# Performance work log

Hardware: AMD Instinct MI355X
Metric: run time of the kernel (lower is better)

Reference implementation:

```python
import jax, jax.numpy as jnp
import numpy as np

EPS = 1e-5

def inorm(x):
    # instance norm over time (last) axis; torch.std is unbiased (ddof=1)
    m = jnp.mean(x, axis=-1, keepdims=True)
    s = jnp.sqrt(jnp.var(x, axis=-1, ddof=1, keepdims=True))
    return (x - m) / (s + EPS)

def tinorm(x):
    # time-wise instance norm: normalize over channel axis (dim=1)
    m = jnp.mean(x, axis=1, keepdims=True)
    s = jnp.sqrt(jnp.var(x, axis=1, ddof=1, keepdims=True))
    return (x - m) / (s + EPS)

def adaptive_norm(src, trg, wq, wk, wv, norm_fn):
    # src, trg: [B,C,T]; wq/wk/wv: [out,in] as in nn.Linear
    temp = src.shape[1] ** 0.5
    q = jnp.einsum('bct,oc->bto', norm_fn(src), wq)        # [B,Ts,C]
    k = jnp.einsum('bct,oc->bto', norm_fn(trg), wk)        # [B,Tt,C]
    v = jnp.einsum('bct,oc->bto', trg, wv)                 # [B,Tt,C]
    attn = jax.nn.softmax(jnp.einsum('bsc,btc->bst', q / temp, k), axis=-1)
    mean = jnp.einsum('bst,btc->bsc', attn, v)             # attn-weighted mean
    var = jax.nn.relu(jnp.einsum('bst,btc->bsc', attn, v * v) - mean * mean)
    mean_c = jnp.mean(mean, axis=1)[:, :, None]            # [B,C,1]
    std_c = jnp.sqrt(jnp.mean(var, axis=1))[:, :, None]    # [B,C,1]
    return std_c * inorm(src) + mean_c

def sap(x, w, b):
    # self-attention pooling over axis 1; x: [B,N,C], w: [C], b: [1]
    a = jax.nn.softmax(jnp.einsum('bnc,c->bn', x, w) + b, axis=-1)
    return jnp.einsum('bnc,bn->bc', x, a)

def setup_inputs():
    key = jax.random.key(0)
    ks = jax.random.split(key, 24)
    B, C, Ts, Tt, S = 4, 512, 2048, 2048, 2048
    sc = 1.0 / np.sqrt(C).astype(np.float32)
    return {
        'src': jax.random.normal(ks[0], (B, C, Ts), jnp.float32),
        'trg': jax.random.normal(ks[1], (B, C, Tt), jnp.float32),
        'means': jax.random.normal(ks[2], (B, S, C), jnp.float32),
        'stds': jax.random.uniform(ks[3], (B, S, C), jnp.float32),
        'wq_t': jax.random.normal(ks[4], (C, C), jnp.float32) * sc,
        'wk_t': jax.random.normal(ks[5], (C, C), jnp.float32) * sc,
        'wv_t': jax.random.normal(ks[6], (C, C), jnp.float32) * sc,
        'wq_c': jax.random.normal(ks[7], (C, C), jnp.float32) * sc,
        'wk_c': jax.random.normal(ks[8], (C, C), jnp.float32) * sc,
        'wv_c': jax.random.normal(ks[9], (C, C), jnp.float32) * sc,
        'conv1_w': jax.random.normal(ks[10], (C, 2 * C), jnp.float32) * sc,
        'conv1_b': jax.random.normal(ks[11], (C,), jnp.float32) * 0.02,
        'conv2_w': jax.random.normal(ks[12], (C, C, 3), jnp.float32) * sc,
        'bn_g': jax.random.uniform(ks[13], (C,), jnp.float32, 0.5, 1.5),
        'bn_b': jax.random.normal(ks[14], (C,), jnp.float32) * 0.05,
        'bn_m': jax.random.normal(ks[15], (C,), jnp.float32) * 0.1,
        'bn_v': jax.random.uniform(ks[16], (C,), jnp.float32, 0.5, 1.5),
        'msap_w': jax.random.normal(ks[17], (C,), jnp.float32) * sc,
        'msap_b': jax.random.normal(ks[18], (1,), jnp.float32) * 0.02,
        'ssap_w': jax.random.normal(ks[19], (C,), jnp.float32) * sc,
        'ssap_b': jax.random.normal(ks[20], (1,), jnp.float32) * 0.02,
    }

def reference(src, trg, means, stds, wq_t, wk_t, wv_t, wq_c, wk_c, wv_c,
              conv1_w, conv1_b, conv2_w, bn_g, bn_b, bn_m, bn_v,
              msap_w, msap_b, ssap_w, ssap_b):
    src1 = adaptive_norm(src, trg, wq_t, wk_t, wv_t, tinorm)   # TAN
    src2 = adaptive_norm(src, trg, wq_c, wk_c, wv_c, inorm)    # CAN
    x = jnp.concatenate([src1, src2], axis=1)                  # [B,2C,T]
    # conv1: kernel_size=1 -> pointwise GEMM
    x = jnp.einsum('bct,oc->bot', x, conv1_w) + conv1_b[None, :, None]
    # conv2: Conv1d(k=3, pad=1, bias=False) + BatchNorm1d(eval) + ReLU
    x = jax.lax.conv_general_dilated(x, conv2_w, (1,), 'SAME',
                                     dimension_numbers=('NCH', 'OIH', 'NCH'))
    x = (x - bn_m[None, :, None]) * jax.lax.rsqrt(bn_v[None, :, None] + EPS)
    x = x * bn_g[None, :, None] + bn_b[None, :, None]
    x = jax.nn.relu(x)
    # GLAN
    mean = sap(means, msap_w, msap_b)[:, :, None]              # [B,C,1]
    std = sap(stds, ssap_w, ssap_b)[:, :, None]                # [B,C,1]
    return inorm(x) * std + mean
```

## Files before the change

kernel.cpp:

```cpp
#include <hip/hip_runtime.h>
#include <cstdint>
#include <cstddef>

#define B_ 4
#define C_ 512
#define T_ 2048
#define S_ 2048
#define EPSF 1e-5f

typedef __bf16 bf16;
typedef __attribute__((ext_vector_type(8))) __bf16 bf16x8;
typedef __attribute__((ext_vector_type(4))) float f32x4;

__device__ __forceinline__ bf16 f2b(float f){ return (bf16)f; }
__device__ __forceinline__ float b2f(bf16 h){ return (float)h; }

__device__ __forceinline__ void gl_lds16(const void* g, void* l){
  __builtin_amdgcn_global_load_lds((__attribute__((address_space(1))) void*)(g),
                                   (__attribute__((address_space(3))) void*)(l), 16, 0, 0);
}

__device__ __forceinline__ float wave_sum(float v){
#pragma unroll
  for (int o = 32; o; o >>= 1) v += __shfl_xor(v, o, 64);
  return v;
}
__device__ __forceinline__ float wave_max(float v){
#pragma unroll
  for (int o = 32; o; o >>= 1) v = fmaxf(v, __shfl_xor(v, o, 64));
  return v;
}

template<int EPI, int TNW, int SWZ>
__global__ void __launch_bounds__(256) gemm_nt(
    const bf16* __restrict__ A, const bf16* __restrict__ Bm, void* __restrict__ Cout,
    int K, int lda, int ldb, int ldc,
    long long sA, long long sB, long long sC, long long sCb,
    int zdivA, int zmodB, int nblk, float scale,
    const float* __restrict__ rs, const float* __restrict__ rsh,
    const float* __restrict__ cbias,
    float* __restrict__ osum, float* __restrict__ osum2, long long sRs)
{
  constexpr int TN = TNW*32;
  __shared__ alignas(16) bf16 lA[128*64];
  __shared__ alignas(16) bf16 lB[TN*64];
  __shared__ float l_sh[EPI == 3 ? 128 : 4];
  const int tid = threadIdx.x;
  int z, m0, n0;
  if (SWZ) {
    const int id = blockIdx.x;
    z = id & 7;
    const int r = id >> 3;
    n0 = (r % nblk) * TN;
    m0 = (r / nblk) * 128;
  } else {
    z = blockIdx.z; m0 = blockIdx.y*128; n0 = blockIdx.x*TN;
  }
  const bf16* Ab = A + (long long)(z / zdivA) * sA;
  const bf16* Bb = Bm + (long long)(z % zmodB) * sB;
  const int lane = tid & 63, wvi = tid >> 6;
  const int wm = wvi >> 1, wn = wvi & 1;

  f32x4 acc[4][TNW] = {};
  f32x4 accL[4] = {};
  bf16x8 vone;
#pragma unroll
  for (int j = 0; j < 8; ++j) vone[j] = f2b(1.f);

  const int lrow = tid >> 3;
  const int lcol = ((tid ^ lrow) & 7) * 8;
  const bf16* pa = Ab + (long long)(m0 + lrow)*lda + lcol;
  const bf16* pb = Bb + (long long)(n0 + lrow)*ldb + lcol;
  char* sa = (char*)lA + tid*16;
  char* sb = (char*)lB + tid*16;

  for (int k0 = 0; k0 < K; k0 += 64) {
#pragma unroll
    for (int it = 0; it < 4; ++it)
      gl_lds16(pa + (long long)it*32*lda + k0, sa + it*4096);
#pragma unroll
    for (int it = 0; it < TNW; ++it)
      gl_lds16(pb + (long long)it*32*ldb + k0, sb + it*4096);
    __syncthreads();
#pragma unroll
    for (int ks = 0; ks < 2; ++ks) {
      const int kq = ks*4 + (lane >> 4);
      bf16x8 af[4], bfr[TNW];
#pragma unroll
      for (int mt = 0; mt < 4; ++mt) {
        int r = wm*64 + mt*16 + (lane & 15);
        af[mt] = *(const bf16x8*)&lA[r*64 + ((kq ^ (r & 7))*8)];
      }
#pragma unroll
      for (int nt = 0; nt < TNW; ++nt) {
        int r = wn*(TNW*16) + nt*16 + (lane & 15);
        bfr[nt] = *(const bf16x8*)&lB[r*64 + ((kq ^ (r & 7))*8)];
      }
#pragma unroll
      for (int mt = 0; mt < 4; ++mt)
#pragma unroll
        for (int nt = 0; nt < TNW; ++nt)
          acc[mt][nt] = __builtin_amdgcn_mfma_f32_16x16x32_bf16(af[mt], bfr[nt], acc[mt][nt], 0, 0, 0);
      if (EPI == 3 && wn == 0) {
#pragma unroll
        for (int mt = 0; mt < 4; ++mt)
          accL[mt] = __builtin_amdgcn_mfma_f32_16x16x32_bf16(af[mt], vone, accL[mt], 0, 0, 0);
      }
    }
    __syncthreads();
  }

  if (EPI == 3) {
    if (wn == 0 && (lane & 15) == 0) {
#pragma unroll
      for (int mt = 0; mt < 4; ++mt)
#pragma unroll
        for (int i = 0; i < 4; ++i)
          l_sh[wm*64 + mt*16 + (lane >> 4)*4 + i] = accL[mt][i];
    }
    __syncthreads();
    if (n0 == 0 && tid < 128)
      ((float*)Cout)[(long long)z*sC + m0 + tid] = l_sh[tid];
    float linv[4][4];
#pragma unroll
    for (int mt = 0; mt < 4; ++mt)
#pragma unroll
      for (int i = 0; i < 4; ++i)
        linv[mt][i] = 1.f / l_sh[wm*64 + mt*16 + (lane >> 4)*4 + i];
    float* red1 = (float*)lA;
    float* red2 = red1 + 4*TNW*16;
    float s1[TNW], s2[TNW];
#pragma unroll
    for (int nt = 0; nt < TNW; ++nt) {
      s1[nt] = 0.f; s2[nt] = 0.f;
#pragma unroll
      for (int mt = 0; mt < 4; ++mt)
#pragma unroll
        for (int i = 0; i < 4; ++i) {
          float v = acc[mt][nt][i] * linv[mt][i];
          s1[nt] += v; s2[nt] += v*v;
        }
      s1[nt] += __shfl_xor(s1[nt], 16, 64);
      s1[nt] += __shfl_xor(s1[nt], 32, 64);
      s2[nt] += __shfl_xor(s2[nt], 16, 64);
      s2[nt] += __shfl_xor(s2[nt], 32, 64);
    }
    if (lane < 16) {
#pragma unroll
      for (int nt = 0; nt < TNW; ++nt) {
        red1[(wvi*TNW + nt)*16 + lane] = s1[nt];
        red2[(wvi*TNW + nt)*16 + lane] = s2[nt];
      }
    }
    __syncthreads();
    if (tid < 2*TN) {
      const int which = tid >= TN;
      const int col = tid - which*TN;
      const int wn2 = col / (TNW*16), rem = col % (TNW*16);
      const float* rr = which ? red2 : red1;
      float v = rr[wn2*(TNW*16) + rem] + rr[(2+wn2)*(TNW*16) + rem];
      float* dst = which ? osum2 : osum;
      atomicAdd(&dst[sCb*z + n0 + col], v);
    }
    return;
  }

  const int cr = (lane >> 4)*4, cc = lane & 15;
#pragma unroll
  for (int mt = 0; mt < 4; ++mt) {
#pragma unroll
    for (int i = 0; i < 4; ++i) {
      const int mm = m0 + wm*64 + mt*16 + cr + i;
      float rsum = 0.f, rsum2 = 0.f;
#pragma unroll
      for (int nt = 0; nt < TNW; ++nt) {
        const int nn = n0 + wn*(TNW*16) + nt*16 + cc;
        float v = acc[mt][nt][i];
        const long long co = sC*z + (long long)mm*ldc + nn;
        if (EPI == 0) {
          v *= scale;
          if (cbias) v += cbias[sCb*z + nn];
          ((bf16*)Cout)[co] = f2b(v);
        } else if (EPI == 2) {
          v = fmaxf(v*rs[mm] + rsh[mm], 0.f);
          ((float*)Cout)[co] = v;
          rsum += v; rsum2 += v*v;
        } else if (EPI == 5) {
          ((bf16*)Cout)[co] = f2b(__expf(v));
        }
      }
      if (EPI == 2) {
        rsum += __shfl_xor(rsum, 1, 64); rsum += __shfl_xor(rsum, 2, 64);
        rsum += __shfl_xor(rsum, 4, 64); rsum += __shfl_xor(rsum, 8, 64);
        rsum2 += __shfl_xor(rsum2, 1, 64); rsum2 += __shfl_xor(rsum2, 2, 64);
        rsum2 += __shfl_xor(rsum2, 4, 64); rsum2 += __shfl_xor(rsum2, 8, 64);
        if (cc == 0) {
          atomicAdd(&osum[(long long)z*sRs + mm], rsum);
          atomicAdd(&osum2[(long long)z*sRs + mm], rsum2);
        }
      }
    }
  }
}

__global__ void __launch_bounds__(256) instats_k(const float* __restrict__ src,
    const float* __restrict__ trg, float* __restrict__ inm, float* __restrict__ ins,
    float* __restrict__ tnm, float* __restrict__ tns)
{
  const int bid = blockIdx.x, tid = threadIdx.x;
  if (bid < 4096) {
    __shared__ float r1[4], r2[4];
    const int row = bid;
    const float* x = (row < B_*C_) ? src + (long long)row*T_
                                   : trg + (long long)(row - B_*C_)*T_;
    float s1 = 0.f, s2 = 0.f;
#pragma unroll
    for (int h = 0; h < 2; ++h) {
      f32x4 v = *(const f32x4*)(x + h*1024 + tid*4);
#pragma unroll
      for (int j = 0; j < 4; ++j){ s1 += v[j]; s2 += v[j]*v[j]; }
    }
    s1 = wave_sum(s1); s2 = wave_sum(s2);
    const int lane = tid & 63, w = tid >> 6;
    if (!lane){ r1[w] = s1; r2[w] = s2; }
    __syncthreads();
    if (tid == 0){
      s1 = r1[0]+r1[1]+r1[2]+r1[3];
      s2 = r2[0]+r2[1]+r2[2]+r2[3];
      float m = s1 * (1.f/T_);
      float var = (s2 - s1*m) * (1.f/(T_-1));
      inm[row] = m; ins[row] = sqrtf(fmaxf(var, 0.f));
    }
  } else {
    __shared__ float r1[4][64], r2[4][64];
    const int cid = bid - 4096;
    const int z = cid >> 5, t0 = (cid & 31)*64;
    const float* X = (z < B_) ? src : trg;
    const int b = z & (B_-1);
    const int tl = tid & 63, cg = tid >> 6;
    float s1 = 0.f, s2 = 0.f;
    for (int c = cg; c < C_; c += 4) {
      float v = X[((long long)b*C_ + c)*T_ + t0 + tl];
      s1 += v; s2 += v*v;
    }
    r1[cg][tl] = s1; r2[cg][tl] = s2;
    __syncthreads();
    if (cg == 0) {
      s1 = r1[0][tl]+r1[1][tl]+r1[2][tl]+r1[3][tl];
      s2 = r2[0][tl]+r2[1][tl]+r2[2][tl]+r2[3][tl];
      float m = s1 * (1.f/C_);
      float var = (s2 - s1*m) * (1.f/(C_-1));
      tnm[z*T_ + t0 + tl] = m;
      tns[z*T_ + t0 + tl] = sqrtf(fmaxf(var, 0.f));
    }
  }
}

__global__ void __launch_bounds__(256) transform_k(const float* __restrict__ src,
    const float* __restrict__ trg,
    const float* __restrict__ tnm, const float* __restrict__ tns,
    const float* __restrict__ inm, const float* __restrict__ ins,
    bf16* __restrict__ NSt, bf16* __restrict__ NSc,
    bf16* __restrict__ NTt, bf16* __restrict__ NTc, bf16* __restrict__ TTr)
{
  __shared__ float tile[32][33];
  const int z = blockIdx.z, t0 = blockIdx.x*32, c0 = blockIdx.y*32;
  const int is_t = z >= B_, b = z & (B_-1);
  const float* X = is_t ? trg : src;
  const int tx = threadIdx.x, ty = threadIdx.y;
#pragma unroll
  for (int r = 0; r < 4; ++r) {
    int ci = ty + r*8;
    tile[ci][tx] = X[((long long)b*C_ + c0 + ci)*T_ + t0 + tx];
  }
  __syncthreads();
#pragma unroll
  for (int r = 0; r < 4; ++r) {
    int tj = ty + r*8, ci = tx;
    float v = tile[ci][tj];
    int gt = t0 + tj, gc = c0 + ci;
    float a = (v - tnm[z*T_ + gt]) / (tns[z*T_ + gt] + EPSF);
    float d = (v - inm[z*C_ + gc]) / (ins[z*C_ + gc] + EPSF);
    long long o = ((long long)b*T_ + gt)*C_ + gc;
    if (is_t) { NTt[o] = f2b(a); NTc[o] = f2b(d); TTr[o] = f2b(v); }
    else      { NSt[o] = f2b(a); NSc[o] = f2b(d); }
  }
}

__global__ void __launch_bounds__(256) softmax_row_k(const float* __restrict__ X, float* __restrict__ O)
{
  __shared__ float red[4];
  const long long row = blockIdx.x;
  const float* x = X + row*T_ + threadIdx.x*8;
  float v[8];
  f32x4 a0 = *(const f32x4*)x;
  f32x4 a1 = *(const f32x4*)(x + 4);
#pragma unroll
  for (int j = 0; j < 4; ++j){ v[j] = a0[j]; v[4+j] = a1[j]; }
  float m = -3.4e38f;
#pragma unroll
  for (int j = 0; j < 8; ++j) m = fmaxf(m, v[j]);
  m = wave_max(m);
  const int lane = threadIdx.x & 63, w = threadIdx.x >> 6;
  if (!lane) red[w] = m;
  __syncthreads();
  m = fmaxf(fmaxf(red[0], red[1]), fmaxf(red[2], red[3]));
  __syncthreads();
  float s = 0.f;
#pragma unroll
  for (int j = 0; j < 8; ++j){ v[j] = __expf(v[j] - m); s += v[j]; }
  s = wave_sum(s);
  if (!lane) red[w] = s;
  __syncthreads();
  s = red[0]+red[1]+red[2]+red[3];
  const float inv = 1.f/s;
  float* o = O + row*T_ + threadIdx.x*8;
#pragma unroll
  for (int j = 0; j < 8; ++j) o[j] = v[j]*inv;
}

__global__ void __launch_bounds__(256) colsum_k(const bf16* __restrict__ P,
    const float* __restrict__ l, float* __restrict__ cs)
{
  __shared__ float linv[32];
  const int id = blockIdx.x;
  const int z = id & 7;
  const long long s0 = (long long)(id >> 3) * 32;
  const int tid = threadIdx.x;
  if (tid < 32) linv[tid] = 1.f / l[(long long)z*S_ + s0 + tid];
  __syncthreads();
  const int t0 = tid*8;
  const bf16* p = P + ((long long)z*S_ + s0)*T_ + t0;
  float a[8] = {};
#pragma unroll 4
  for (int s = 0; s < 32; ++s) {
    bf16x8 v = *(const bf16x8*)(p + (long long)s*T_);
    const float w = linv[s];
#pragma unroll
    for (int j = 0; j < 8; ++j) a[j] += b2f(v[j]) * w;
  }
#pragma unroll
  for (int j = 0; j < 8; ++j) atomicAdd(&cs[z*T_ + t0 + j], a[j]);
}

__global__ void __launch_bounds__(256) vv_fin_k(const float* __restrict__ cs,
    const bf16* __restrict__ VT, const float* __restrict__ msum,
    const float* __restrict__ m2sum, float* __restrict__ meanc, float* __restrict__ stdc)
{
  __shared__ float r1[4];
  const int c = blockIdx.x, z = blockIdx.y;
  const int tid = threadIdx.x;
  const bf16* vr = VT + ((long long)z*C_ + c)*T_ + tid*8;
  const float* w = cs + z*T_ + tid*8;
  bf16x8 v = *(const bf16x8*)vr;
  f32x4 w0 = *(const f32x4*)w;
  f32x4 w1 = *(const f32x4*)(w + 4);
  float a = 0.f;
#pragma unroll
  for (int j = 0; j < 4; ++j) {
    float f0 = b2f(v[j]), f1 = b2f(v[4+j]);
    a += w0[j]*f0*f0 + w1[j]*f1*f1;
  }
  a = wave_sum(a);
  const int lane = tid & 63, wq = tid >> 6;
  if (!lane) r1[wq] = a;
  __syncthreads();
  if (tid == 0){
    a = r1[0]+r1[1]+r1[2]+r1[3];
    const int idx = z*C_ + c;
    meanc[idx] = msum[idx] * (1.f/S_);
    float var = (a - m2sum[idx]) * (1.f/S_);
    stdc[idx] = sqrtf(fmaxf(var, 0.f));
  }
}

__global__ void __launch_bounds__(256) weff_k(const float* __restrict__ w1,
    const float* __restrict__ b1, const float* __restrict__ sdt, const float* __restrict__ sdc,
    const float* __restrict__ mct, const float* __restrict__ mcc,
    bf16* __restrict__ Weff, float* __restrict__ beff)
{
  __shared__ float r1[4];
  const int o = blockIdx.x, b = blockIdx.y;
  float accb = 0.f;
  for (int c = threadIdx.x; c < C_; c += 256) {
    float wa = w1[o*2*C_ + c], wb = w1[o*2*C_ + C_ + c];
    Weff[((long long)(b*C_ + o))*C_ + c] = f2b(wa*sdt[b*C_+c] + wb*sdc[b*C_+c]);
    accb += wa*mct[b*C_+c] + wb*mcc[b*C_+c];
  }
  accb = wave_sum(accb);
  const int lane = threadIdx.x & 63, w = threadIdx.x >> 6;
  if (!lane) r1[w] = accb;
  __syncthreads();
  if (threadIdx.x == 0) beff[b*C_ + o] = b1[o] + r1[0]+r1[1]+r1[2]+r1[3];
}

__global__ void __launch_bounds__(256) prep_k(
    const float* __restrict__ a0, const float* __restrict__ a1,
    const float* __restrict__ a2, const float* __restrict__ a3,
    const float* __restrict__ a4, const float* __restrict__ a5,
    bf16* __restrict__ WQb,
    const float* __restrict__ w2, const float* __restrict__ g,
    const float* __restrict__ be, const float* __restrict__ mu,
    const float* __restrict__ va, bf16* __restrict__ W2r,
    float* __restrict__ bnsc, float* __restrict__ bnsh,
    bf16* __restrict__ x1p, float* __restrict__ zbase)
{
  const int bid = blockIdx.x, tid = threadIdx.x;
  if (bid < 6144) {
    const int i = bid*256 + tid;
    const int slot = i >> 18;
    const float* srcs[6] = {a0,a1,a2,a3,a4,a5};
    const float sc = (slot < 2) ? 0.044194173824159216f : 1.f;
    WQb[i] = f2b(srcs[slot][i & 262143] * sc);
  } else if (bid < 6656) {
    const int o = bid - 6144;
    for (int c = tid; c < C_; c += 256)
#pragma unroll
      for (int dt = 0; dt < 3; ++dt)
        W2r[(long long)o*3*C_ + dt*C_ + c] = f2b(w2[((long long)o*C_ + c)*3 + dt]);
    if (tid == 0) {
      float s = g[o] * rsqrtf(va[o] + EPSF);
      bnsc[o] = s;
      bnsh[o] = be[o] - mu[o]*s;
    }
  } else if (bid < 6672) {
    const int i = (bid - 6656)*256 + tid;
    const int b = i >> 10, rem = i & 1023;
    const long long row = (rem >> 9) ? (T_+1) : 0;
    const int c = rem & (C_-1);
    x1p[((long long)b*(T_+2) + row)*C_ + c] = f2b(0.f);
  } else {
    zbase[(bid - 6672)*256 + tid] = 0.f;
  }
}

__global__ void __launch_bounds__(256) sap_logit_k(const float* __restrict__ means,
    const float* __restrict__ stds, const float* __restrict__ mw, const float* __restrict__ sw,
    const float* __restrict__ mb, const float* __restrict__ sb, float* __restrict__ out)
{
  const int tid = threadIdx.x;
  const int n = blockIdx.x*4 + (tid >> 6);
  const int z = blockIdx.y;
  const int sel = z >= B_, b = z & (B_-1);
  const float* x = sel ? stds : means;
  const float* w = sel ? sw : mw;
  const int lane = tid & 63;
  const float* p = x + ((long long)b*S_ + n)*C_ + lane*8;
  f32x4 p0 = *(const f32x4*)p;
  f32x4 p1 = *(const f32x4*)(p + 4);
  f32x4 w0 = *(const f32x4*)(w + lane*8);
  f32x4 w1 = *(const f32x4*)(w + lane*8 + 4);
  float a = 0.f;
#pragma unroll
  for (int j = 0; j < 4; ++j) a += p0[j]*w0[j] + p1[j]*w1[j];
  a = wave_sum(a);
  if (!lane) out[z*S_ + n] = a + (sel ? sb[0] : mb[0]);
}

__global__ void __launch_bounds__(256) sap_wsum_k(const float* __restrict__ means,
    const float* __restrict__ stds, const float* __restrict__ a, float* __restrict__ out)
{
  const int c = blockIdx.x*256 + threadIdx.x;
  const int z = blockIdx.z;
  const int sel = z >= B_, b = z & (B_-1);
  const float* x = sel ? stds : means;
  const long long n0 = (long long)blockIdx.y*64;
  const float* p = x + ((long long)b*S_ + n0)*C_ + c;
  const float* aw = a + z*S_ + n0;
  float acc = 0.f;
#pragma unroll 4
  for (int n = 0; n < 64; ++n) acc += p[(long long)n*C_] * aw[n];
  atomicAdd(&out[z*C_ + c], acc);
}

__global__ void __launch_bounds__(256) final_k(const float* __restrict__ y,
    const float* __restrict__ ysum, const float* __restrict__ y2sum,
    const float* __restrict__ sapms, float* __restrict__ out)
{
  const long long i = (long long)(blockIdx.x*256 + threadIdx.x) * 4;
  const long long r = i >> 11;
  const float s1 = ysum[r], s2 = y2sum[r];
  const float m = s1 * (1.f/T_);
  const float var = (s2 - s1*m) * (1.f/(T_-1));
  const float inv = 1.f/(sqrtf(fmaxf(var, 0.f)) + EPSF);
  const float mn = sapms[r], sd = sapms[B_*C_ + r];
  const f32x4 v = *(const f32x4*)(y + i);
  f32x4 o;
#pragma unroll
  for (int j = 0; j < 4; ++j) o[j] = (v[j] - m)*inv*sd + mn;
  *(f32x4*)(out + i) = o;
}

extern "C" void kernel_launch(void* const* d_in, const int* in_sizes, int n_in,
                              void* d_out, int out_size, void* d_ws, size_t ws_size,
                              hipStream_t stream)
{
  (void)in_sizes; (void)n_in; (void)out_size; (void)ws_size;
  const float* src    = (const float*)d_in[0];
  const float* trg    = (const float*)d_in[1];
  const float* means  = (const float*)d_in[2];
  const float* stds   = (const float*)d_in[3];
  const float* conv1w = (const float*)d_in[10];
  const float* conv1b = (const float*)d_in[11];
  const float* conv2w = (const float*)d_in[12];
  const float* bn_g   = (const float*)d_in[13];
  const float* bn_b   = (const float*)d_in[14];
  const float* bn_m   = (const float*)d_in[15];
  const float* bn_v   = (const float*)d_in[16];
  const float* msap_w = (const float*)d_in[17];
  const float* msap_b = (const float*)d_in[18];
  const float* ssap_w = (const float*)d_in[19];
  const float* ssap_b = (const float*)d_in[20];

  const long long BTC = (long long)B_*T_*C_;

  char* p = (char*)d_ws;
  auto take = [&](size_t n)->char*{ char* r = p; p += (n + 255) & ~(size_t)255; return r; };

  bf16* NSc = (bf16*)take(BTC*2);
  bf16* P2  = (bf16*)take((size_t)2*B_*S_*T_*2);
  bf16* NSt = P2;
  bf16* NTc = P2 + BTC;
  bf16* NTt = P2 + 2*BTC;
  bf16* TTr = P2 + 3*BTC;
  bf16* QK4 = (bf16*)take((size_t)4*BTC*2);
  bf16* VT2 = (bf16*)take((size_t)2*BTC*2);
  bf16* WQb = (bf16*)take((size_t)6*C_*C_*2);
  bf16* Weff= (bf16*)take((size_t)B_*C_*C_*2);
  bf16* W2r = (bf16*)take((size_t)C_*3*C_*2);
  bf16* x1p = (bf16*)take((size_t)B_*(T_+2)*C_*2);
  float* y  = (float*)take((size_t)B_*C_*T_*4);
  float* colsum = (float*)take(2*B_*T_*4);
  float* msum   = (float*)take(2*B_*C_*4);
  float* m2sum  = (float*)take(2*B_*C_*4);
  float* sapms  = (float*)take(2*B_*C_*4);
  float* lrow   = (float*)take(2*B_*S_*4);
  float* ysum   = (float*)take(B_*C_*4);
  float* y2sum  = (float*)take(B_*C_*4);
  float* tnm = (float*)take(2*B_*T_*4);
  float* tns = (float*)take(2*B_*T_*4);
  float* inm = (float*)take(2*B_*C_*4);
  float* ins = (float*)take(2*B_*C_*4);
  float* meanc = (float*)take(2*B_*C_*4);
  float* stdc  = (float*)take(2*B_*C_*4);
  float* beff  = (float*)take(B_*C_*4);
  float* bnsc  = (float*)take(C_*4);
  float* bnsh  = (float*)take(C_*4);
  float* sapl  = (float*)take(2*B_*S_*4);
  float* sapa  = (float*)take(2*B_*S_*4);

  dim3 blk(256);

  prep_k<<<6864, blk, 0, stream>>>((const float*)d_in[7], (const float*)d_in[4],
      (const float*)d_in[8], (const float*)d_in[5], (const float*)d_in[9],
      (const float*)d_in[6], WQb, conv2w, bn_g, bn_b, bn_m, bn_v, W2r, bnsc, bnsh,
      x1p, colsum);
  instats_k<<<4352, blk, 0, stream>>>(src, trg, inm, ins, tnm, tns);
  transform_k<<<dim3(T_/32, C_/32, 2*B_), dim3(32,8), 0, stream>>>(src, trg,
      tnm, tns, inm, ins, NSt, NSc, NTt, NTc, TTr);

  gemm_nt<0,4,0><<<dim3(C_/128, (B_*T_)/128, 4), blk, 0, stream>>>(NSc, WQb, QK4,
      C_, C_, C_, C_, BTC, (long long)C_*C_, BTC, 0, 1, 8, 0, 1.f,
      nullptr, nullptr, nullptr, nullptr, nullptr, 0);
  gemm_nt<0,2,1><<<1024, blk, 0, stream>>>(WQb + (size_t)4*C_*C_, TTr, VT2,
      C_, C_, C_, T_, (long long)C_*C_, (long long)T_*C_, (long long)C_*T_, 0, 4, 4, 32, 1.f,
      nullptr, nullptr, nullptr, nullptr, nullptr, 0);
  gemm_nt<5,4,1><<<2048, blk, 0, stream>>>(QK4, QK4 + 2*BTC, P2,
      C_, C_, C_, T_, (long long)T_*C_, (long long)T_*C_, (long long)S_*T_, 0, 1, 8, 16, 1.f,
      nullptr, nullptr, nullptr, nullptr, nullptr, 0);
  gemm_nt<3,4,1><<<512, blk, 0, stream>>>(P2, VT2, lrow,
      T_, T_, T_, 0, (long long)S_*T_, (long long)C_*T_, S_, C_, 1, 8, 4, 1.f,
      nullptr, nullptr, nullptr, msum, m2sum, 0);
  colsum_k<<<512, blk, 0, stream>>>(P2, lrow, colsum);
  vv_fin_k<<<dim3(C_, 2*B_), blk, 0, stream>>>(colsum, VT2, msum, m2sum, meanc, stdc);

  weff_k<<<dim3(C_, B_), blk, 0, stream>>>(conv1w, conv1b,
      stdc + B_*C_, stdc, meanc + B_*C_, meanc, Weff, beff);
  gemm_nt<0,2,0><<<dim3(C_/64, T_/128, B_), blk, 0, stream>>>(NSc, Weff, x1p + C_,
      C_, C_, C_, C_, (long long)T_*C_, (long long)C_*C_, (long long)(T_+2)*C_, C_,
      1, 8, 0, 1.f, nullptr, nullptr, beff, nullptr, nullptr, 0);
  gemm_nt<2,2,0><<<dim3(T_/64, C_/128, B_), blk, 0, stream>>>(W2r, x1p, y,
      3*C_, 3*C_, C_, T_, 0, (long long)(T_+2)*C_, (long long)C_*T_, 0,
      1, 8, 0, 1.f, bnsc, bnsh, nullptr, ysum, y2sum, C_);

  sap_logit_k<<<dim3(S_/4, 2*B_), blk, 0, stream>>>(means, stds, msap_w, ssap_w,
      msap_b, ssap_b, sapl);
  softmax_row_k<<<2*B_, blk, 0, stream>>>(sapl, sapa);
  sap_wsum_k<<<dim3(C_/256, S_/64, 2*B_), blk, 0, stream>>>(means, stds, sapa, sapms);

  final_k<<<4096, blk, 0, stream>>>(y, ysum, y2sum, sapms, (float*)d_out);
}
```

Baseline: 465.8 us.

## Fold SAP pooling into prep/transform/GEMM tails and merge stats into prep

```diff
diff --git a/kernel.cpp b/kernel.cpp
--- a/kernel.cpp
+++ b/kernel.cpp
@@ -23,11 +23,6 @@
 __device__ __forceinline__ float wave_sum(float v){
 #pragma unroll
   for (int o = 32; o; o >>= 1) v += __shfl_xor(v, o, 64);
-  return v;
-}
-__device__ __forceinline__ float wave_max(float v){
-#pragma unroll
-  for (int o = 32; o; o >>= 1) v = fmaxf(v, __shfl_xor(v, o, 64));
   return v;
 }
 
@@ -39,13 +34,30 @@
     int zdivA, int zmodB, int nblk, float scale,
     const float* __restrict__ rs, const float* __restrict__ rsh,
     const float* __restrict__ cbias,
-    float* __restrict__ osum, float* __restrict__ osum2, long long sRs)
+    float* __restrict__ osum, float* __restrict__ osum2, long long sRs,
+    int tailBase, const float* __restrict__ tailE)
 {
   constexpr int TN = TNW*32;
+  const int tid = threadIdx.x;
+  if (SWZ && tailBase && (int)blockIdx.x >= tailBase) {
+    const int rel = blockIdx.x - tailBase;
+    const int zz = rel & 7;
+    const int rb = rel >> 3;
+    const int c  = (rb & 1)*256 + tid;
+    const int n0b = (rb >> 1) * 64;
+    const int selp = zz >= B_, b = zz & (B_-1);
+    const float* x = selp ? rsh : rs;
+    const float* e = tailE + (long long)zz*S_ + n0b;
+    const float* px = x + ((long long)b*S_ + n0b)*C_ + c;
+    float accT = 0.f;
+#pragma unroll 4
+    for (int n = 0; n < 64; ++n) accT += px[(long long)n*C_] * e[n];
+    atomicAdd(&osum[zz*C_ + c], accT);
+    return;
+  }
   __shared__ alignas(16) bf16 lA[128*64];
   __shared__ alignas(16) bf16 lB[TN*64];
   __shared__ float l_sh[EPI == 3 ? 128 : 4];
-  const int tid = threadIdx.x;
   int z, m0, n0;
   if (SWZ) {
     const int id = blockIdx.x;
@@ -203,14 +215,50 @@
   }
 }
 
-__global__ void __launch_bounds__(256) instats_k(const float* __restrict__ src,
-    const float* __restrict__ trg, float* __restrict__ inm, float* __restrict__ ins,
+__global__ void __launch_bounds__(256) prep_k(
+    const float* __restrict__ a0, const float* __restrict__ a1,
+    const float* __restrict__ a2, const float* __restrict__ a3,
+    const float* __restrict__ a4, const float* __restrict__ a5,
+    bf16* __restrict__ WQb,
+    const float* __restrict__ w2, const float* __restrict__ g,
+    const float* __restrict__ be, const float* __restrict__ mu,
+    const float* __restrict__ va, bf16* __restrict__ W2r,
+    float* __restrict__ bnsc, float* __restrict__ bnsh,
+    bf16* __restrict__ x1p, float* __restrict__ zbase,
+    const float* __restrict__ src, const float* __restrict__ trg,
+    float* __restrict__ inm, float* __restrict__ ins,
     float* __restrict__ tnm, float* __restrict__ tns)
 {
   const int bid = blockIdx.x, tid = threadIdx.x;
-  if (bid < 4096) {
+  if (bid < 6144) {
+    const int i = bid*256 + tid;
+    const int slot = i >> 18;
+    const float* srcs[6] = {a0,a1,a2,a3,a4,a5};
+    const float sc = (slot < 2) ? 0.044194173824159216f : 1.f;
+    WQb[i] = f2b(srcs[slot][i & 262143] * sc);
+  } else if (bid < 6656) {
+    const int o = bid - 6144;
+    for (int c = tid; c < C_; c += 256)
+#pragma unroll
+      for (int dt = 0; dt < 3; ++dt)
+        W2r[(long long)o*3*C_ + dt*C_ + c] = f2b(w2[((long long)o*C_ + c)*3 + dt]);
+    if (tid == 0) {
+      float s = g[o] * rsqrtf(va[o] + EPSF);
+      bnsc[o] = s;
+      bnsh[o] = be[o] - mu[o]*s;
+    }
+  } else if (bid < 6672) {
+    const int i = (bid - 6656)*256 + tid;
+    const int b = i >> 10, rem = i & 1023;
+    const long long row = (rem >> 9) ? (T_+1) : 0;
+    const int c = rem & (C_-1);
+    x1p[((long long)b*(T_+2) + row)*C_ + c] = f2b(0.f);
+  } else if (bid < 6865) {
+    const int i = (bid - 6672)*256 + tid;
+    if (i < 49216) zbase[i] = 0.f;
+  } else if (bid < 10961) {
     __shared__ float r1[4], r2[4];
-    const int row = bid;
+    const int row = bid - 6865;
     const float* x = (row < B_*C_) ? src + (long long)row*T_
                                    : trg + (long long)(row - B_*C_)*T_;
     float s1 = 0.f, s2 = 0.f;
@@ -232,8 +280,8 @@
       inm[row] = m; ins[row] = sqrtf(fmaxf(var, 0.f));
     }
   } else {
-    __shared__ float r1[4][64], r2[4][64];
-    const int cid = bid - 4096;
+    __shared__ float c1[4][64], c2[4][64];
+    const int cid = bid - 10961;
     const int z = cid >> 5, t0 = (cid & 31)*64;
     const float* X = (z < B_) ? src : trg;
     const int b = z & (B_-1);
@@ -243,11 +291,11 @@
       float v = X[((long long)b*C_ + c)*T_ + t0 + tl];
       s1 += v; s2 += v*v;
     }
-    r1[cg][tl] = s1; r2[cg][tl] = s2;
+    c1[cg][tl] = s1; c2[cg][tl] = s2;
     __syncthreads();
     if (cg == 0) {
-      s1 = r1[0][tl]+r1[1][tl]+r1[2][tl]+r1[3][tl];
-      s2 = r2[0][tl]+r2[1][tl]+r2[2][tl]+r2[3][tl];
+      s1 = c1[0][tl]+c1[1][tl]+c1[2][tl]+c1[3][tl];
+      s2 = c2[0][tl]+c2[1][tl]+c2[2][tl]+c2[3][tl];
       float m = s1 * (1.f/C_);
       float var = (s2 - s1*m) * (1.f/(C_-1));
       tnm[z*T_ + t0 + tl] = m;
@@ -261,8 +309,37 @@
     const float* __restrict__ tnm, const float* __restrict__ tns,
     const float* __restrict__ inm, const float* __restrict__ ins,
     bf16* __restrict__ NSt, bf16* __restrict__ NSc,
-    bf16* __restrict__ NTt, bf16* __restrict__ NTc, bf16* __restrict__ TTr)
-{
+    bf16* __restrict__ NTt, bf16* __restrict__ NTc, bf16* __restrict__ TTr,
+    const float* __restrict__ means, const float* __restrict__ stds,
+    const float* __restrict__ mw, const float* __restrict__ sw,
+    const float* __restrict__ mb, const float* __restrict__ sb,
+    float* __restrict__ sapl, float* __restrict__ sapD)
+{
+  const int ftid = threadIdx.y*32 + threadIdx.x;
+  if (blockIdx.z >= 8) {
+    __shared__ float se[4];
+    const int rel = (blockIdx.z - 8)*1024 + blockIdx.y*64 + blockIdx.x;
+    const int z = rel >> 9;
+    const int n = (rel & 511)*4 + (ftid >> 6);
+    const int sel = z >= B_, b = z & (B_-1);
+    const float* x = sel ? stds : means;
+    const float* w = sel ? sw : mw;
+    const int lane = ftid & 63;
+    const float* p = x + ((long long)b*S_ + n)*C_ + lane*8;
+    f32x4 p0 = *(const f32x4*)p;
+    f32x4 p1 = *(const f32x4*)(p + 4);
+    f32x4 w0 = *(const f32x4*)(w + lane*8);
+    f32x4 w1 = *(const f32x4*)(w + lane*8 + 4);
+    float a = 0.f;
+#pragma unroll
+    for (int j = 0; j < 4; ++j) a += p0[j]*w0[j] + p1[j]*w1[j];
+    a = wave_sum(a);
+    float e = __expf(a + (sel ? sb[0] : mb[0]));
+    if (!lane) { sapl[z*S_ + n] = e; se[ftid >> 6] = e; }
+    __syncthreads();
+    if (ftid == 0) atomicAdd(&sapD[z], se[0]+se[1]+se[2]+se[3]);
+    return;
+  }
   __shared__ float tile[32][33];
   const int z = blockIdx.z, t0 = blockIdx.x*32, c0 = blockIdx.y*32;
   const int is_t = z >= B_, b = z & (B_-1);
@@ -285,38 +362,6 @@
     if (is_t) { NTt[o] = f2b(a); NTc[o] = f2b(d); TTr[o] = f2b(v); }
     else      { NSt[o] = f2b(a); NSc[o] = f2b(d); }
   }
-}
-
-__global__ void __launch_bounds__(256) softmax_row_k(const float* __restrict__ X, float* __restrict__ O)
-{
-  __shared__ float red[4];
-  const long long row = blockIdx.x;
-  const float* x = X + row*T_ + threadIdx.x*8;
-  float v[8];
-  f32x4 a0 = *(const f32x4*)x;
-  f32x4 a1 = *(const f32x4*)(x + 4);
-#pragma unroll
-  for (int j = 0; j < 4; ++j){ v[j] = a0[j]; v[4+j] = a1[j]; }
-  float m = -3.4e38f;
-#pragma unroll
-  for (int j = 0; j < 8; ++j) m = fmaxf(m, v[j]);
-  m = wave_max(m);
-  const int lane = threadIdx.x & 63, w = threadIdx.x >> 6;
-  if (!lane) red[w] = m;
-  __syncthreads();
-  m = fmaxf(fmaxf(red[0], red[1]), fmaxf(red[2], red[3]));
-  __syncthreads();
-  float s = 0.f;
-#pragma unroll
-  for (int j = 0; j < 8; ++j){ v[j] = __expf(v[j] - m); s += v[j]; }
-  s = wave_sum(s);
-  if (!lane) red[w] = s;
-  __syncthreads();
-  s = red[0]+red[1]+red[2]+red[3];
-  const float inv = 1.f/s;
-  float* o = O + row*T_ + threadIdx.x*8;
-#pragma unroll
-  for (int j = 0; j < 8; ++j) o[j] = v[j]*inv;
 }
 
 __global__ void __launch_bounds__(256) colsum_k(const bf16* __restrict__ P,
@@ -394,96 +439,20 @@
   if (threadIdx.x == 0) beff[b*C_ + o] = b1[o] + r1[0]+r1[1]+r1[2]+r1[3];
 }
 
-__global__ void __launch_bounds__(256) prep_k(
-    const float* __restrict__ a0, const float* __restrict__ a1,
-    const float* __restrict__ a2, const float* __restrict__ a3,
-    const float* __restrict__ a4, const float* __restrict__ a5,
-    bf16* __restrict__ WQb,
-    const float* __restrict__ w2, const float* __restrict__ g,
-    const float* __restrict__ be, const float* __restrict__ mu,
-    const float* __restrict__ va, bf16* __restrict__ W2r,
-    float* __restrict__ bnsc, float* __restrict__ bnsh,
-    bf16* __restrict__ x1p, float* __restrict__ zbase)
-{
-  const int bid = blockIdx.x, tid = threadIdx.x;
-  if (bid < 6144) {
-    const int i = bid*256 + tid;
-    const int slot = i >> 18;
-    const float* srcs[6] = {a0,a1,a2,a3,a4,a5};
-    const float sc = (slot < 2) ? 0.044194173824159216f : 1.f;
-    WQb[i] = f2b(srcs[slot][i & 262143] * sc);
-  } else if (bid < 6656) {
-    const int o = bid - 6144;
-    for (int c = tid; c < C_; c += 256)
-#pragma unroll
-      for (int dt = 0; dt < 3; ++dt)
-        W2r[(long long)o*3*C_ + dt*C_ + c] = f2b(w2[((long long)o*C_ + c)*3 + dt]);
-    if (tid == 0) {
-      float s = g[o] * rsqrtf(va[o] + EPSF);
-      bnsc[o] = s;
-      bnsh[o] = be[o] - mu[o]*s;
-    }
-  } else if (bid < 6672) {
-    const int i = (bid - 6656)*256 + tid;
-    const int b = i >> 10, rem = i & 1023;
-    const long long row = (rem >> 9) ? (T_+1) : 0;
-    const int c = rem & (C_-1);
-    x1p[((long long)b*(T_+2) + row)*C_ + c] = f2b(0.f);
-  } else {
-    zbase[(bid - 6672)*256 + tid] = 0.f;
-  }
-}
-
-__global__ void __launch_bounds__(256) sap_logit_k(const float* __restrict__ means,
-    const float* __restrict__ stds, const float* __restrict__ mw, const float* __restrict__ sw,
-    const float* __restrict__ mb, const float* __restrict__ sb, float* __restrict__ out)
-{
-  const int tid = threadIdx.x;
-  const int n = blockIdx.x*4 + (tid >> 6);
-  const int z = blockIdx.y;
-  const int sel = z >= B_, b = z & (B_-1);
-  const float* x = sel ? stds : means;
-  const float* w = sel ? sw : mw;
-  const int lane = tid & 63;
-  const float* p = x + ((long long)b*S_ + n)*C_ + lane*8;
-  f32x4 p0 = *(const f32x4*)p;
-  f32x4 p1 = *(const f32x4*)(p + 4);
-  f32x4 w0 = *(const f32x4*)(w + lane*8);
-  f32x4 w1 = *(const f32x4*)(w + lane*8 + 4);
-  float a = 0.f;
-#pragma unroll
-  for (int j = 0; j < 4; ++j) a += p0[j]*w0[j] + p1[j]*w1[j];
-  a = wave_sum(a);
-  if (!lane) out[z*S_ + n] = a + (sel ? sb[0] : mb[0]);
-}
-
-__global__ void __launch_bounds__(256) sap_wsum_k(const float* __restrict__ means,
-    const float* __restrict__ stds, const float* __restrict__ a, float* __restrict__ out)
-{
-  const int c = blockIdx.x*256 + threadIdx.x;
-  const int z = blockIdx.z;
-  const int sel = z >= B_, b = z & (B_-1);
-  const float* x = sel ? stds : means;
-  const long long n0 = (long long)blockIdx.y*64;
-  const float* p = x + ((long long)b*S_ + n0)*C_ + c;
-  const float* aw = a + z*S_ + n0;
-  float acc = 0.f;
-#pragma unroll 4
-  for (int n = 0; n < 64; ++n) acc += p[(long long)n*C_] * aw[n];
-  atomicAdd(&out[z*C_ + c], acc);
-}
-
 __global__ void __launch_bounds__(256) final_k(const float* __restrict__ y,
     const float* __restrict__ ysum, const float* __restrict__ y2sum,
-    const float* __restrict__ sapms, float* __restrict__ out)
+    const float* __restrict__ sapms, const float* __restrict__ sapD,
+    float* __restrict__ out)
 {
   const long long i = (long long)(blockIdx.x*256 + threadIdx.x) * 4;
   const long long r = i >> 11;
+  const int b = (int)(r >> 9);
   const float s1 = ysum[r], s2 = y2sum[r];
   const float m = s1 * (1.f/T_);
   const float var = (s2 - s1*m) * (1.f/(T_-1));
   const float inv = 1.f/(sqrtf(fmaxf(var, 0.f)) + EPSF);
-  const float mn = sapms[r], sd = sapms[B_*C_ + r];
+  const float mn = sapms[r] / sapD[b];
+  const float sd = sapms[B_*C_ + r] / sapD[B_ + b];
   const f32x4 v = *(const f32x4*)(y + i);
   f32x4 o;
 #pragma unroll
@@ -537,6 +506,7 @@
   float* lrow   = (float*)take(2*B_*S_*4);
   float* ysum   = (float*)take(B_*C_*4);
   float* y2sum  = (float*)take(B_*C_*4);
+  float* sapD   = (float*)take(8*4);
   float* tnm = (float*)take(2*B_*T_*4);
   float* tns = (float*)take(2*B_*T_*4);
   float* inm = (float*)take(2*B_*C_*4);
@@ -547,30 +517,29 @@
   float* bnsc  = (float*)take(C_*4);
   float* bnsh  = (float*)take(C_*4);
   float* sapl  = (float*)take(2*B_*S_*4);
-  float* sapa  = (float*)take(2*B_*S_*4);
 
   dim3 blk(256);
 
-  prep_k<<<6864, blk, 0, stream>>>((const float*)d_in[7], (const float*)d_in[4],
+  prep_k<<<11217, blk, 0, stream>>>((const float*)d_in[7], (const float*)d_in[4],
       (const float*)d_in[8], (const float*)d_in[5], (const float*)d_in[9],
       (const float*)d_in[6], WQb, conv2w, bn_g, bn_b, bn_m, bn_v, W2r, bnsc, bnsh,
-      x1p, colsum);
-  instats_k<<<4352, blk, 0, stream>>>(src, trg, inm, ins, tnm, tns);
-  transform_k<<<dim3(T_/32, C_/32, 2*B_), dim3(32,8), 0, stream>>>(src, trg,
-      tnm, tns, inm, ins, NSt, NSc, NTt, NTc, TTr);
+      x1p, colsum, src, trg, inm, ins, tnm, tns);
+  transform_k<<<dim3(T_/32, C_/32, 12), dim3(32,8), 0, stream>>>(src, trg,
+      tnm, tns, inm, ins, NSt, NSc, NTt, NTc, TTr,
+      means, stds, msap_w, ssap_w, msap_b, ssap_b, sapl, sapD);
 
   gemm_nt<0,4,0><<<dim3(C_/128, (B_*T_)/128, 4), blk, 0, stream>>>(NSc, WQb, QK4,
       C_, C_, C_, C_, BTC, (long long)C_*C_, BTC, 0, 1, 8, 0, 1.f,
-      nullptr, nullptr, nullptr, nullptr, nullptr, 0);
-  gemm_nt<0,2,1><<<1024, blk, 0, stream>>>(WQb + (size_t)4*C_*C_, TTr, VT2,
+      nullptr, nullptr, nullptr, nullptr, nullptr, 0, 0, nullptr);
+  gemm_nt<0,2,1><<<1536, blk, 0, stream>>>(WQb + (size_t)4*C_*C_, TTr, VT2,
       C_, C_, C_, T_, (long long)C_*C_, (long long)T_*C_, (long long)C_*T_, 0, 4, 4, 32, 1.f,
-      nullptr, nullptr, nullptr, nullptr, nullptr, 0);
+      means, stds, nullptr, sapms, nullptr, 0, 1024, sapl);
   gemm_nt<5,4,1><<<2048, blk, 0, stream>>>(QK4, QK4 + 2*BTC, P2,
       C_, C_, C_, T_, (long long)T_*C_, (long long)T_*C_, (long long)S_*T_, 0, 1, 8, 16, 1.f,
-      nullptr, nullptr, nullptr, nullptr, nullptr, 0);
-  gemm_nt<3,4,1><<<512, blk, 0, stream>>>(P2, VT2, lrow,
-      T_, T_, T_, 0, (long long)S_*T_, (long long)C_*T_, S_, C_, 1, 8, 4, 1.f,
-      nullptr, nullptr, nullptr, msum, m2sum, 0);
+      nullptr, nullptr, nullptr, nullptr, nullptr, 0, 0, nullptr);
+  gemm_nt<3,2,1><<<1024, blk, 0, stream>>>(P2, VT2, lrow,
+      T_, T_, T_, 0, (long long)S_*T_, (long long)C_*T_, S_, C_, 1, 8, 8, 1.f,
+      nullptr, nullptr, nullptr, msum, m2sum, 0, 0, nullptr);
   colsum_k<<<512, blk, 0, stream>>>(P2, lrow, colsum);
   vv_fin_k<<<dim3(C_, 2*B_), blk, 0, stream>>>(colsum, VT2, msum, m2sum, meanc, stdc);
 
@@ -578,15 +547,10 @@
       stdc + B_*C_, stdc, meanc + B_*C_, meanc, Weff, beff);
   gemm_nt<0,2,0><<<dim3(C_/64, T_/128, B_), blk, 0, stream>>>(NSc, Weff, x1p + C_,
       C_, C_, C_, C_, (long long)T_*C_, (long long)C_*C_, (long long)(T_+2)*C_, C_,
-      1, 8, 0, 1.f, nullptr, nullptr, beff, nullptr, nullptr, 0);
+      1, 8, 0, 1.f, nullptr, nullptr, beff, nullptr, nullptr, 0, 0, nullptr);
   gemm_nt<2,2,0><<<dim3(T_/64, C_/128, B_), blk, 0, stream>>>(W2r, x1p, y,
       3*C_, 3*C_, C_, T_, 0, (long long)(T_+2)*C_, (long long)C_*T_, 0,
-      1, 8, 0, 1.f, bnsc, bnsh, nullptr, ysum, y2sum, C_);
-
-  sap_logit_k<<<dim3(S_/4, 2*B_), blk, 0, stream>>>(means, stds, msap_w, ssap_w,
-      msap_b, ssap_b, sapl);
-  softmax_row_k<<<2*B_, blk, 0, stream>>>(sapl, sapa);
-  sap_wsum_k<<<dim3(C_/256, S_/64, 2*B_), blk, 0, stream>>>(means, stds, sapa, sapms);
-
-  final_k<<<4096, blk, 0, stream>>>(y, ysum, y2sum, sapms, (float*)d_out);
-}
+      1, 8, 0, 1.f, bnsc, bnsh, nullptr, ysum, y2sum, C_, 0, nullptr);
+
+  final_k<<<4096, blk, 0, stream>>>(y, ysum, y2sum, sapms, sapD, (float*)d_out);
+}
```

New measurement: 526.6 us. 1.13x slower.
